# Optimization experiments

Measured on AMD Instinct MI355X. Metric: run time of the kernel, lower is better.

Reference implementation:

```python
import jax, jax.numpy as jnp
import numpy as np

N_IN = 262144      # input points
N_OUT = 65536      # output voxels
NBR = 32           # neighbors per voxel (uniform ragged list here)
E = N_OUT * NBR    # total edges
CIN = 32
COUT = 32
K = 3 + 1          # kernel_size = [4,4,4]
KV = K * K * K     # 64 kernel bins
EPS = 1e-8


def window_poly6(r):
    # poly6 window on normalized distance r in [0,1]
    return jnp.clip(1.0 - r * r, 0.0, 1.0) ** 3


def ball_to_cube_radial(p):
    # radially map unit ball to unit cube [-1,1]^3 (Open3D 'ball_to_cube_radial')
    n2 = jnp.sqrt(jnp.sum(p * p, axis=-1, keepdims=True) + 1e-12)
    ninf = jnp.max(jnp.abs(p), axis=-1, keepdims=True)
    scale = jnp.where(ninf > 1e-8, n2 / jnp.maximum(ninf, 1e-8), 0.0)
    return jnp.clip(p * scale, -1.0, 1.0)


def setup_inputs() -> dict:
    key = jax.random.key(0)
    ks = jax.random.split(key, 8)
    feats = jax.random.normal(ks[0], (N_IN, CIN), jnp.float32)
    inp_points = jax.random.uniform(ks[1], (N_IN, 3), jnp.float32)
    out_points = jax.random.uniform(ks[2], (N_OUT, 3), jnp.float32)
    out_extents = jnp.array([0.2], jnp.float32)  # voxel size
    scale_compat = jax.random.uniform(ks[3], (E,), jnp.float32)
    neighbors_index = jax.random.randint(ks[4], (E,), 0, N_IN).astype(jnp.int64)
    neighbors_row_splits = (jnp.arange(N_OUT + 1) * NBR).astype(jnp.int64)
    neighbors_distance = jax.random.uniform(ks[5], (E,), jnp.float32)
    # learned params of the ContinuousConv: kernel [4,4,4,Cin,Cout] flattened, bias
    W = jax.random.normal(ks[6], (KV, CIN, COUT), jnp.float32) * 0.05
    bias = jnp.zeros((COUT,), jnp.float32)
    return dict(feats=feats, inp_points=inp_points, out_points=out_points,
                out_extents=out_extents, scale_compat=scale_compat,
                neighbors_index=neighbors_index,
                neighbors_row_splits=neighbors_row_splits,
                neighbors_distance=neighbors_distance, W=W, bias=bias)


def reference(feats, inp_points, out_points, out_extents, scale_compat,
              neighbors_index, neighbors_row_splits, neighbors_distance,
              W, bias):
    # edge -> output-voxel index from ragged row splits
    out_idx = jnp.searchsorted(neighbors_row_splits, jnp.arange(E), side='right') - 1
    # per-neighbor importance (the CConvAggregationBlock weighting)
    a = scale_compat * window_poly6(neighbors_distance)
    # relative positions normalized to the voxel extent (ball radius = extent/2)
    rel = (inp_points[neighbors_index] - out_points[out_idx]) * (2.0 / out_extents[0])
    cube = ball_to_cube_radial(rel)                      # [E,3] in [-1,1]
    u = jnp.clip((cube + 1.0) * 0.5 * (K - 1), 0.0, K - 1)
    i0 = jnp.clip(jnp.floor(u), 0.0, K - 2)
    t = u - i0                                           # trilinear fractions [E,3]
    i0 = i0.astype(jnp.int32)
    fg = feats[neighbors_index]                          # gathered features [E,Cin]
    # accumulate importance-weighted features into per-voxel kernel bins
    B = jnp.zeros((N_OUT * KV, CIN), feats.dtype)
    for dx in (0, 1):
        for dy in (0, 1):
            for dz in (0, 1):
                w = ((t[:, 0] if dx else 1.0 - t[:, 0]) *
                     (t[:, 1] if dy else 1.0 - t[:, 1]) *
                     (t[:, 2] if dz else 1.0 - t[:, 2]))
                kflat = ((i0[:, 0] + dx) * K + (i0[:, 1] + dy)) * K + (i0[:, 2] + dz)
                B = B.at[out_idx * KV + kflat].add((w * a)[:, None] * fg)
    # kernel contraction + importance normalization (normalize=True) + bias + relu
    y = jnp.einsum('nkc,kcd->nd', B.reshape(N_OUT, KV, CIN), W)
    denom = jax.ops.segment_sum(a, out_idx, num_segments=N_OUT)
    y = y / jnp.maximum(denom, EPS)[:, None] + bias
    return jax.nn.relu(y)
```

## Files before the change

### kernel.cpp

```cpp
#include <hip/hip_runtime.h>
#include <hip/hip_bf16.h>


typedef unsigned short u16;
typedef unsigned int   u32;
typedef __attribute__((ext_vector_type(4))) float f32x4;
typedef __attribute__((ext_vector_type(8))) short short8;

#define NOUT    65536
#define VX      8
#define THREADS 512
#define EPW     256
#define NWG     (NOUT / VX)
#define BSTRIDE 2052
#define VROWB   (BSTRIDE * 4)
#define BL_BYTES (VX * VROWB)

#define OFF_W   BL_BYTES
#define OFF_D   (OFF_W + 8*EPW*4)
#define OFF_BCA (OFF_D + 8*EPW*2)
#define OFF_FB  (OFF_BCA + EPW*4)
#define OFF_DEN (OFF_FB + EPW*4)
#define SMEM_BYTES (OFF_DEN + 64)

__global__ void prep_w_kernel(const float* __restrict__ W,
                              u16* __restrict__ wt_hi,
                              u16* __restrict__ wt_lo) {
  int t  = blockIdx.x * 256 + threadIdx.x;
  int kr = t >> 5;
  int d  = t & 31;
  float w = W[t];
  unsigned u = __float_as_uint(w);
  u16 hi = (u16)(u >> 16);
  float rem = w - __uint_as_float(u & 0xFFFF0000u);
  u16 lo = (u16)(__float_as_uint(rem) >> 16);
  wt_hi[d * 2048 + kr] = hi;
  wt_lo[d * 2048 + kr] = lo;
}

__launch_bounds__(THREADS, 4)
__global__ void cconv_kernel(const float* __restrict__ feats,
                             const float* __restrict__ inp_points,
                             const float* __restrict__ out_points,
                             const float* __restrict__ out_extents,
                             const float* __restrict__ scale_compat,
                             const int*   __restrict__ nbr_idx,
                             const int*   __restrict__ row_splits,
                             const float* __restrict__ nbr_dist,
                             const float* __restrict__ bias,
                             const u16*   __restrict__ wt_hi,
                             const u16*   __restrict__ wt_lo,
                             float*       __restrict__ out) {
  extern __shared__ __align__(16) char smem[];
  float* wls   = (float*)(smem + OFF_W);
  float* Yp    = wls;
  u16*   dlt   = (u16*)(smem + OFF_D);
  u32*   bca   = (u32*)(smem + OFF_BCA);
  int*   fbase = (int*)(smem + OFF_FB);
  float* den   = (float*)(smem + OFF_DEN);

  const int tid  = threadIdx.x;
  const int wg   = blockIdx.x;
  const int lane = tid & 63;
  const int wv   = tid >> 6;

  {
    f32x4 z = {0.f, 0.f, 0.f, 0.f};
    for (int i = tid; i < (BL_BYTES / 16); i += THREADS)
      ((f32x4*)smem)[i] = z;
  }
  if (tid < VX) den[tid] = 0.f;

  if (tid < EPW) {
    const bool is64 = (row_splits[1] == 0);
    int e  = tid;
    int v  = e >> 5;
    int gv = (wg << 3) + v;
    int ge = (wg << 8) + e;
    int idx = nbr_idx[is64 ? (ge << 1) : ge];
    float dist = nbr_dist[ge];
    float sc   = scale_compat[ge];
    float om = 1.f - dist * dist;
    om = fminf(fmaxf(om, 0.f), 1.f);
    float a = sc * om * om * om;
    float inv = 2.f / out_extents[0];
    float ox = out_points[gv * 3 + 0];
    float oy = out_points[gv * 3 + 1];
    float oz = out_points[gv * 3 + 2];
    float rx = (inp_points[idx * 3 + 0] - ox) * inv;
    float ry = (inp_points[idx * 3 + 1] - oy) * inv;
    float rz = (inp_points[idx * 3 + 2] - oz) * inv;
    float n2   = sqrtf(rx * rx + ry * ry + rz * rz + 1e-12f);
    float ninf = fmaxf(fabsf(rx), fmaxf(fabsf(ry), fabsf(rz)));
    float scl  = (ninf > 1e-8f) ? (n2 / ninf) : 0.f;
    float cx = fminf(fmaxf(rx * scl, -1.f), 1.f);
    float cy = fminf(fmaxf(ry * scl, -1.f), 1.f);
    float cz = fminf(fmaxf(rz * scl, -1.f), 1.f);
    float ux = fminf(fmaxf((cx + 1.f) * 1.5f, 0.f), 3.f);
    float uy = fminf(fmaxf((cy + 1.f) * 1.5f, 0.f), 3.f);
    float uz = fminf(fmaxf((cz + 1.f) * 1.5f, 0.f), 3.f);
    float fx = fminf(floorf(ux), 2.f);
    float fy = fminf(floorf(uy), 2.f);
    float fz = fminf(floorf(uz), 2.f);
    float tx = ux - fx, ty = uy - fy, tz = uz - fz;
    int ix = (int)fx, iy = (int)fy, iz = (int)fz;
    float X1 = tx * a, X0 = a - X1;
    float Y1 = ty,     Y0 = 1.f - ty;
    float Z1 = tz,     Z0 = 1.f - tz;
    float p00 = X0 * Y0, p01 = X0 * Y1, p10 = X1 * Y0, p11 = X1 * Y1;
    float wc[8];
    wc[0] = p00 * Z0; wc[1] = p00 * Z1; wc[2] = p01 * Z0; wc[3] = p01 * Z1;
    wc[4] = p10 * Z0; wc[5] = p10 * Z1; wc[6] = p11 * Z0; wc[7] = p11 * Z1;
    const int DLT[8] = {0, 128, 512, 640, 2048, 2176, 2560, 2688};
    int kb = (ix * 4 + iy) * 4 + iz;
    u32 bb = (u32)(v * VROWB + (kb << 7));
    int nc = 0;
    #pragma unroll
    for (int k = 0; k < 8; ++k) {
      if (wc[k] != 0.f) {
        wls[nc * EPW + e] = wc[k];
        dlt[nc * EPW + e] = (u16)DLT[k];
        ++nc;
      }
    }
    bca[e]   = bb | ((u32)nc << 16);
    fbase[e] = idx << 5;
    atomicAdd(&den[v], a);
  }
  __syncthreads();

  {
    const int c  = tid & 31;
    const int e0 = tid >> 5;
    float fg[16];
    u32   bcn[16];
    #pragma unroll
    for (int it = 0; it < 16; ++it) {
      int e = (it << 4) + e0;
      bcn[it] = bca[e];
      fg[it]  = feats[fbase[e] + c];
    }
    #pragma unroll
    for (int it = 0; it < 16; ++it) {
      int e   = (it << 4) + e0;
      u32 m   = bcn[it];
      int nc  = (int)(m >> 16);
      u32 base = (m & 0xFFFFu) + ((u32)c << 2);
      float f = fg[it];
      for (int j = 0; j < nc; ++j) {
        float w = wls[j * EPW + e];
        u32   d = dlt[j * EPW + e];
        atomicAdd((float*)(smem + base + d), w * f);
      }
    }
  }
  __syncthreads();

  f32x4 acc0 = {0.f, 0.f, 0.f, 0.f};
  f32x4 acc1 = {0.f, 0.f, 0.f, 0.f};
  {
    int v16 = lane & 15;
    int q   = lane >> 4;
    const char* arow = smem + (size_t)(v16 & 7) * VROWB;
    #pragma unroll
    for (int b = 0; b < 8; ++b) {
      int bin = (wv << 3) + b;
      const float* ap = (const float*)(arow + (bin << 7) + (q << 5));
      f32x4 a0 = *(const f32x4*)ap;
      f32x4 a1 = *(const f32x4*)(ap + 4);
      short8 ahi, alo;
      #pragma unroll
      for (int j = 0; j < 4; ++j) {
        unsigned u0 = __float_as_uint(a0[j]);
        ahi[j] = (short)(u0 >> 16);
        float r0 = a0[j] - __uint_as_float(u0 & 0xFFFF0000u);
        alo[j] = (short)(__float_as_uint(r0) >> 16);
        unsigned u1 = __float_as_uint(a1[j]);
        ahi[j + 4] = (short)(u1 >> 16);
        float r1 = a1[j] - __uint_as_float(u1 & 0xFFFF0000u);
        alo[j + 4] = (short)(__float_as_uint(r1) >> 16);
      }
      int krow = (bin << 5) + (q << 3);
      {
        int d = v16;
        short8 wh = *(const short8*)(wt_hi + d * 2048 + krow);
        short8 wl = *(const short8*)(wt_lo + d * 2048 + krow);
        acc0 = __builtin_amdgcn_mfma_f32_16x16x32_bf16(ahi, wh, acc0, 0, 0, 0);
        acc0 = __builtin_amdgcn_mfma_f32_16x16x32_bf16(ahi, wl, acc0, 0, 0, 0);
        acc0 = __builtin_amdgcn_mfma_f32_16x16x32_bf16(alo, wh, acc0, 0, 0, 0);
      }
      {
        int d = v16 + 16;
        short8 wh = *(const short8*)(wt_hi + d * 2048 + krow);
        short8 wl = *(const short8*)(wt_lo + d * 2048 + krow);
        acc1 = __builtin_amdgcn_mfma_f32_16x16x32_bf16(ahi, wh, acc1, 0, 0, 0);
        acc1 = __builtin_amdgcn_mfma_f32_16x16x32_bf16(ahi, wl, acc1, 0, 0, 0);
        acc1 = __builtin_amdgcn_mfma_f32_16x16x32_bf16(alo, wh, acc1, 0, 0, 0);
      }
    }
  }
  __syncthreads();

  {
    if (lane < 32) {
      float* yp = Yp + (wv << 8);
      int v0 = (lane >> 4) << 2;
      int d0 = lane & 15;
      #pragma unroll
      for (int r = 0; r < 4; ++r) {
        yp[(v0 + r) * 32 + d0]      = acc0[r];
        yp[(v0 + r) * 32 + 16 + d0] = acc1[r];
      }
    }
  }
  __syncthreads();

  if (tid < EPW) {
    float s = 0.f;
    #pragma unroll
    for (int w = 0; w < 8; ++w) s += Yp[(w << 8) + tid];
    int v = tid >> 5;
    int d = tid & 31;
    float dn = fmaxf(den[v], 1e-8f);
    float y = s / dn + bias[d];
    out[(wg << 8) + tid] = fmaxf(y, 0.f);
  }
}

extern "C" void kernel_launch(void* const* d_in, const int* in_sizes, int n_in,
                              void* d_out, int out_size, void* d_ws, size_t ws_size,
                              hipStream_t stream) {
  const float* feats        = (const float*)d_in[0];
  const float* inp_points   = (const float*)d_in[1];
  const float* out_points   = (const float*)d_in[2];
  const float* out_extents  = (const float*)d_in[3];
  const float* scale_compat = (const float*)d_in[4];
  const int*   nbr_idx      = (const int*)d_in[5];
  const int*   row_splits   = (const int*)d_in[6];
  const float* nbr_dist     = (const float*)d_in[7];
  const float* W            = (const float*)d_in[8];
  const float* bias         = (const float*)d_in[9];

  u16* wt_hi = (u16*)d_ws;
  u16* wt_lo = wt_hi + 2048 * 32;

  static_assert(SMEM_BYTES <= 81920, "LDS over 2-per-CU budget");
  (void)hipFuncSetAttribute((const void*)cconv_kernel,
                            hipFuncAttributeMaxDynamicSharedMemorySize,
                            SMEM_BYTES);

  prep_w_kernel<<<256, 256, 0, stream>>>(W, wt_hi, wt_lo);
  cconv_kernel<<<NWG, THREADS, SMEM_BYTES, stream>>>(
      feats, inp_points, out_points, out_extents, scale_compat, nbr_idx,
      row_splits, nbr_dist, bias, wt_hi, wt_lo, (float*)d_out);
}
```

Baseline: 648.7 us.

## Halve voxels per workgroup, vectorize scatter, encode corner mask, shuffle-reduce denominators

Each workgroup now handles 4 voxels (128 edges) instead of 8, which roughly halves LDS use so more workgroups fit per CU. The per-corner offset table in LDS is replaced by a bitmask packed into the edge descriptor and decoded with ctz. Feature gathers become float4 loads, and each thread scatters 4 channels for two edges. The shared-memory atomic for the denominator becomes a wavefront shuffle reduction, and one barrier before the partial-result write is removed. In exchange, half of the MFMA rows now hold duplicated voxels, so matrix work per output doubles, and the kernel launches twice as many workgroups.

Result: no change. 637.8 us, median of 2 (-1.7%).

```diff
diff --git a/kernel.cpp b/kernel.cpp
--- a/kernel.cpp
+++ b/kernel.cpp
@@ -8,20 +8,19 @@
 typedef __attribute__((ext_vector_type(8))) short short8;
 
 #define NOUT    65536
-#define VX      8
+#define VX      4
 #define THREADS 512
-#define EPW     256
+#define EPW     128
 #define NWG     (NOUT / VX)
 #define BSTRIDE 2052
 #define VROWB   (BSTRIDE * 4)
 #define BL_BYTES (VX * VROWB)
 
 #define OFF_W   BL_BYTES
-#define OFF_D   (OFF_W + 8*EPW*4)
-#define OFF_BCA (OFF_D + 8*EPW*2)
+#define OFF_BCA (OFF_W + 8*EPW*4)
 #define OFF_FB  (OFF_BCA + EPW*4)
 #define OFF_DEN (OFF_FB + EPW*4)
-#define SMEM_BYTES (OFF_DEN + 64)
+#define SMEM_BYTES (OFF_DEN + 16)
 
 __global__ void prep_w_kernel(const float* __restrict__ W,
                               u16* __restrict__ wt_hi,
@@ -38,7 +37,7 @@
   wt_lo[d * 2048 + kr] = lo;
 }
 
-__launch_bounds__(THREADS, 4)
+__launch_bounds__(THREADS, 8)
 __global__ void cconv_kernel(const float* __restrict__ feats,
                              const float* __restrict__ inp_points,
                              const float* __restrict__ out_points,
@@ -54,7 +53,6 @@
   extern __shared__ __align__(16) char smem[];
   float* wls   = (float*)(smem + OFF_W);
   float* Yp    = wls;
-  u16*   dlt   = (u16*)(smem + OFF_D);
   u32*   bca   = (u32*)(smem + OFF_BCA);
   int*   fbase = (int*)(smem + OFF_FB);
   float* den   = (float*)(smem + OFF_DEN);
@@ -69,14 +67,13 @@
     for (int i = tid; i < (BL_BYTES / 16); i += THREADS)
       ((f32x4*)smem)[i] = z;
   }
-  if (tid < VX) den[tid] = 0.f;
 
   if (tid < EPW) {
     const bool is64 = (row_splits[1] == 0);
     int e  = tid;
     int v  = e >> 5;
-    int gv = (wg << 3) + v;
-    int ge = (wg << 8) + e;
+    int gv = (wg << 2) + v;
+    int ge = (wg << 7) + e;
     int idx = nbr_idx[is64 ? (ge << 1) : ge];
     float dist = nbr_dist[ge];
     float sc   = scale_compat[ge];
@@ -111,46 +108,55 @@
     float wc[8];
     wc[0] = p00 * Z0; wc[1] = p00 * Z1; wc[2] = p01 * Z0; wc[3] = p01 * Z1;
     wc[4] = p10 * Z0; wc[5] = p10 * Z1; wc[6] = p11 * Z0; wc[7] = p11 * Z1;
-    const int DLT[8] = {0, 128, 512, 640, 2048, 2176, 2560, 2688};
     int kb = (ix * 4 + iy) * 4 + iz;
     u32 bb = (u32)(v * VROWB + (kb << 7));
-    int nc = 0;
+    int nc = 0; u32 mask = 0;
     #pragma unroll
     for (int k = 0; k < 8; ++k) {
       if (wc[k] != 0.f) {
         wls[nc * EPW + e] = wc[k];
-        dlt[nc * EPW + e] = (u16)DLT[k];
+        mask |= (1u << k);
         ++nc;
       }
     }
-    bca[e]   = bb | ((u32)nc << 16);
+    bca[e]   = bb | (mask << 16) | ((u32)nc << 24);
     fbase[e] = idx << 5;
-    atomicAdd(&den[v], a);
+    float s = a;
+    s += __shfl_xor(s, 1);
+    s += __shfl_xor(s, 2);
+    s += __shfl_xor(s, 4);
+    s += __shfl_xor(s, 8);
+    s += __shfl_xor(s, 16);
+    if ((lane & 31) == 0) den[v] = s;
   }
   __syncthreads();
 
   {
-    const int c  = tid & 31;
-    const int e0 = tid >> 5;
-    float fg[16];
-    u32   bcn[16];
-    #pragma unroll
-    for (int it = 0; it < 16; ++it) {
-      int e = (it << 4) + e0;
-      bcn[it] = bca[e];
-      fg[it]  = feats[fbase[e] + c];
-    }
-    #pragma unroll
-    for (int it = 0; it < 16; ++it) {
-      int e   = (it << 4) + e0;
-      u32 m   = bcn[it];
-      int nc  = (int)(m >> 16);
-      u32 base = (m & 0xFFFFu) + ((u32)c << 2);
-      float f = fg[it];
+    const int c4 = (tid & 7) << 2;
+    const int eA = (tid >> 3);
+    const int eB = eA + 64;
+    u32 mA = bca[eA], mB = bca[eB];
+    int fA = fbase[eA], fB = fbase[eB];
+    f32x4 gA = *(const f32x4*)&feats[fA + c4];
+    f32x4 gB = *(const f32x4*)&feats[fB + c4];
+    #pragma unroll 2
+    for (int it = 0; it < 2; ++it) {
+      int   e    = it ? eB : eA;
+      u32   m    = it ? mB : mA;
+      f32x4 g    = it ? gB : gA;
+      u32   base = (m & 0xFFFFu) + ((u32)c4 << 2);
+      u32   mask = (m >> 16) & 0xFFu;
+      int   nc   = (int)(m >> 24);
       for (int j = 0; j < nc; ++j) {
         float w = wls[j * EPW + e];
-        u32   d = dlt[j * EPW + e];
-        atomicAdd((float*)(smem + base + d), w * f);
+        int   k = __builtin_ctz(mask);
+        mask &= mask - 1;
+        u32 d = ((k & 1) << 7) | ((k & 2) << 8) | ((k & 4) << 9);
+        float* p = (float*)(smem + base + d);
+        atomicAdd(p + 0, w * g[0]);
+        atomicAdd(p + 1, w * g[1]);
+        atomicAdd(p + 2, w * g[2]);
+        atomicAdd(p + 3, w * g[3]);
       }
     }
   }
@@ -161,7 +167,7 @@
   {
     int v16 = lane & 15;
     int q   = lane >> 4;
-    const char* arow = smem + (size_t)(v16 & 7) * VROWB;
+    const char* arow = smem + (size_t)(v16 & 3) * VROWB;
     #pragma unroll
     for (int b = 0; b < 8; ++b) {
       int bin = (wv << 3) + b;
@@ -199,18 +205,13 @@
       }
     }
   }
-  __syncthreads();
-
-  {
-    if (lane < 32) {
-      float* yp = Yp + (wv << 8);
-      int v0 = (lane >> 4) << 2;
-      int d0 = lane & 15;
-      #pragma unroll
-      for (int r = 0; r < 4; ++r) {
-        yp[(v0 + r) * 32 + d0]      = acc0[r];
-        yp[(v0 + r) * 32 + 16 + d0] = acc1[r];
-      }
+
+  if (lane < 16) {
+    float* yp = Yp + (wv << 7);
+    #pragma unroll
+    for (int r = 0; r < 4; ++r) {
+      yp[r * 32 + lane]      = acc0[r];
+      yp[r * 32 + 16 + lane] = acc1[r];
     }
   }
   __syncthreads();
@@ -218,12 +219,12 @@
   if (tid < EPW) {
     float s = 0.f;
     #pragma unroll
-    for (int w = 0; w < 8; ++w) s += Yp[(w << 8) + tid];
+    for (int w = 0; w < 8; ++w) s += Yp[(w << 7) + tid];
     int v = tid >> 5;
     int d = tid & 31;
     float dn = fmaxf(den[v], 1e-8f);
     float y = s / dn + bias[d];
-    out[(wg << 8) + tid] = fmaxf(y, 0.f);
+    out[(wg << 7) + tid] = fmaxf(y, 0.f);
   }
 }
 
@@ -244,7 +245,7 @@
   u16* wt_hi = (u16*)d_ws;
   u16* wt_lo = wt_hi + 2048 * 32;
 
-  static_assert(SMEM_BYTES <= 81920, "LDS over 2-per-CU budget");
+  static_assert(SMEM_BYTES <= 40960, "LDS over 4-per-CU budget");
   (void)hipFuncSetAttribute((const void*)cconv_kernel,
                             hipFuncAttributeMaxDynamicSharedMemorySize,
                             SMEM_BYTES);
```
